# Optimization experiments

Measured on AMD Instinct MI355X. Metric: run time of the kernel, lower is better.

## Reference

```python
import jax, jax.numpy as jnp
import numpy as np

NUM_FIELDS = 24
FIELD_DIM = 2000
VOCAB = NUM_FIELDS * FIELD_DIM  # sum(field_dims) = 48000
EMBED_DIM = 64
H1, H2 = 64, 32
NUM_INTERACTIONS = 16
BATCH = 4096


def setup_inputs() -> dict:
    key = jax.random.key(0)
    ks = jax.random.split(key, 12)
    s = 0.05  # xavier-ish scale
    return {
        "x": jax.random.randint(ks[0], (BATCH, NUM_FIELDS), 0, FIELD_DIM, dtype=jnp.int32),
        # per-field embedding tables stacked: (num_fields, vocab, embed_dim)
        "tables": jax.random.normal(ks[1], (NUM_FIELDS, VOCAB, EMBED_DIM), jnp.float32) * s,
        "fc_w": jax.random.normal(ks[2], (VOCAB, 1), jnp.float32) * s,
        "fc_b": jnp.zeros((1,), jnp.float32),
        "w1": jax.random.normal(ks[3], (2 * EMBED_DIM, H1), jnp.float32) * s,
        "b1": jnp.zeros((H1,), jnp.float32),
        "w2": jax.random.normal(ks[4], (H1, H2), jnp.float32) * s,
        "b2": jnp.zeros((H2,), jnp.float32),
        "w3": jax.random.normal(ks[5], (H2, 1), jnp.float32) * s,
        "b3": jnp.zeros((1,), jnp.float32),
        "proj_w": jax.random.normal(ks[6], (EMBED_DIM, 1), jnp.float32) * s,
        "proj_b": jnp.zeros((1,), jnp.float32),
        "bias": jnp.zeros((1,), jnp.float32),
    }


def reference(x, tables, fc_w, fc_b, w1, b1, w2, b2, w3, b3, proj_w, proj_b, bias):
    offsets = jnp.arange(NUM_FIELDS, dtype=x.dtype) * FIELD_DIM  # cumsum of equal field_dims
    idx = x + offsets[None, :]  # (B, F)

    # FeaturesLinear: first-order term, (B, 1)
    linear_part = fc_w[idx].sum(axis=1) + fc_b

    # FeaturesEmbedding: per-field table lookup -> (B, F, D)
    emb = tables[jnp.arange(NUM_FIELDS)[None, :], idx]

    # FeatureInteractionDetector: all i<j pairs, concat, score with MLP
    iu, ju = jnp.triu_indices(NUM_FIELDS, k=1)  # (P,), P = F*(F-1)/2
    pair_emb = jnp.concatenate([emb[:, iu], emb[:, ju]], axis=-1)  # (B, P, 2D)
    h = jax.nn.relu(pair_emb @ w1 + b1)
    h = jax.nn.relu(h @ w2 + b2)
    scores = (h @ w3 + b3)[..., 0]  # (B, P)

    # topk over batch-mean scores, gather per-sample scores and pair indices
    _, top = jax.lax.top_k(scores.mean(axis=0), NUM_INTERACTIONS)  # (K,)
    sel_scores = scores[:, top]  # (B, K)
    sel_i, sel_j = iu[top], ju[top]

    # FeatureCrossing: elementwise product of selected pairs, score-weighted sum, project
    crossed = emb[:, sel_i] * emb[:, sel_j]  # (B, K, D)
    summed = jnp.sum(crossed * sel_scores[..., None], axis=1)  # (B, D)
    crossed_part = summed @ proj_w + proj_b  # (B, 1)

    out = linear_part + crossed_part + bias  # (B, 1)
    return out[:, 0]
```

## Files before the change

kernel.cpp:

```cpp
#include <hip/hip_runtime.h>
#include <stdint.h>

#define NF 24
#define FD 2000
#define VOCABSZ 48000
#define ED 64
#define H1D 64
#define H2D 32
#define NPAIR 276
#define BATCH 4096
#define NSEL 16
#define NTILE 256
#define PBASE 49152

typedef _Float16 f16x8 __attribute__((ext_vector_type(8)));
typedef _Float16 f16x2 __attribute__((ext_vector_type(2)));
typedef float f32x4 __attribute__((ext_vector_type(4)));

union U4 { f16x8 v; uint32_t u[4]; uint4 q; };
union H2U { f16x2 h; uint32_t u; };

__device__ __forceinline__ uint32_t pkrtz(float lo, float hi){
  uint32_t r; asm("v_cvt_pkrtz_f16_f32 %0, %1, %2" : "=v"(r) : "v"(lo), "v"(hi)); return r;
}
__device__ __forceinline__ uint32_t pk_add(uint32_t a, uint32_t b){
  uint32_t r; asm("v_pk_add_f16 %0, %1, %2" : "=v"(r) : "v"(a), "v"(b)); return r;
}
__device__ __forceinline__ uint32_t pk_mul(uint32_t a, uint32_t b){
  uint32_t r; asm("v_pk_mul_f16 %0, %1, %2" : "=v"(r) : "v"(a), "v"(b)); return r;
}
__device__ __forceinline__ uint32_t pk_relu(uint32_t a){
  uint32_t r; asm("v_pk_max_f16 %0, %1, %2" : "=v"(r) : "v"(a), "v"(0u)); return r;
}
__device__ __forceinline__ float fdot2(uint32_t a, uint32_t b, float c){
  H2U ua, ub; ua.u = a; ub.u = b;
  return __builtin_amdgcn_fdot2(ua.h, ub.h, c, false);
}
#define DPP_ADD(v, ctrl) \
  (v) += __int_as_float(__builtin_amdgcn_update_dpp(0, __float_as_int(v), (ctrl), 0xF, 0xF, true))

__global__ __launch_bounds__(1024) void k_pair(
    const int* __restrict__ x, const float* __restrict__ tables,
    const float* __restrict__ w1, const float* __restrict__ b1,
    const float* __restrict__ w2, const float* __restrict__ b2,
    const float* __restrict__ w3, const float* __restrict__ b3,
    const float* __restrict__ proj_w,
    float* __restrict__ sgT, float* __restrict__ part){
  __shared__ __align__(16) char smem[147456];
  const int tid  = threadIdx.x;
  const int bt   = blockIdx.x;
  const int lane = tid & 63;
  const int w    = tid >> 6;
  const int n    = lane & 15;
  const int kg   = lane >> 4;

  const int half = w >> 3;
  const int oq   = (w >> 1) & 3;
  const int fg   = w & 1;
  const int isPt = (half == 0);
  const float b3v = b3[0];

  const int o = 16*oq + n;
  U4 wp0, wp1;
  {
    const float* wsrc = w1 + (size_t)(isPt ? 0 : ED)*H1D + o;
    #pragma unroll
    for(int j=0;j<8;j++) wp0.v[j] = (_Float16)wsrc[(kg*8+j)*H1D];
    #pragma unroll
    for(int j=0;j<8;j++) wp1.v[j] = (_Float16)wsrc[(32+kg*8+j)*H1D];
  }
  const float b1v = isPt ? b1[o] : 0.f;

  U4 wf[2][2];
  #pragma unroll
  for(int kh=0;kh<2;kh++)
    #pragma unroll
    for(int nh=0;nh<2;nh++)
      #pragma unroll
      for(int q2=0;q2<4;q2++){
        float lo = w2[(kg*8 + 2*q2     + 32*kh)*H2D + n + 16*nh];
        float hi = w2[(kg*8 + 2*q2 + 1 + 32*kh)*H2D + n + 16*nh];
        wf[kh][nh].u[q2] = pkrtz(lo, hi);
      }
  float b2r[2][4], w3r[2][4];
  #pragma unroll
  for(int oh=0;oh<2;oh++)
    #pragma unroll
    for(int r=0;r<4;r++){
      b2r[oh][r] = b2[16*oh + kg*4 + r];
      w3r[oh][r] = w3[16*oh + kg*4 + r];
    }

  uint32_t pw2[8];
  #pragma unroll
  for(int j=0;j<8;j++) pw2[j] = pkrtz(proj_w[kg*16 + 2*j], proj_w[kg*16 + 2*j + 1]);

  #pragma unroll
  for(int i=0;i<3;i++){
    int c = i*1024 + tid;
    int rid = c >> 3;
    int qc = c & 7;
    int f = rid >> 4, b = rid & 15;
    int xv = x[(bt*16 + b)*NF + f];
    const float4* rp = (const float4*)(tables + ((size_t)f*VOCABSZ + (size_t)f*FD + (size_t)xv)*ED + qc*8);
    float4 v0 = rp[0], v1 = rp[1];
    uint4 pk;
    pk.x = pkrtz(v0.x, v0.y); pk.y = pkrtz(v0.z, v0.w);
    pk.z = pkrtz(v1.x, v1.y); pk.w = pkrtz(v1.z, v1.w);
    uint32_t db = ((uint32_t)(f*2048 + b*128 + qc*16)) ^ ((uint32_t)(b&7)<<4);
    *(uint4*)(smem + db) = pk;
  }
  __syncthreads();

  {
    const uint32_t rswz = ((uint32_t)(n&7))<<4;
    const int slab0 = isPt ? 0 : 24;
    for(int ff=0; ff<12; ff++){
      int f = fg*12 + ff;
      U4 a0, a1;
      a0.q = *(const uint4*)(smem + (((uint32_t)(f*2048 + n*128      + kg*16)) ^ rswz));
      a1.q = *(const uint4*)(smem + (((uint32_t)(f*2048 + n*128 + 64 + kg*16)) ^ rswz));
      f32x4 acc = {b1v, b1v, b1v, b1v};
      acc = __builtin_amdgcn_mfma_f32_16x16x32_f16(a0.v, wp0.v, acc, 0,0,0);
      acc = __builtin_amdgcn_mfma_f32_16x16x32_f16(a1.v, wp1.v, acc, 0,0,0);
      int sl = slab0 + f;
      #pragma unroll
      for(int r=0;r<4;r++){
        int bo = kg*4 + r;
        uint32_t db = ((uint32_t)(PBASE + sl*2048 + bo*128 + o*2)) ^ (((uint32_t)(bo&7))<<4);
        *(_Float16*)(smem + db) = (_Float16)acc[r];
      }
    }
  }
  __syncthreads();

  {
    int p0, np;
    if(w < 4){ np = 18; p0 = w*18; } else { np = 17; p0 = 72 + (w-4)*17; }
    int ii = 0, rem = p0;
    while(rem >= (NF-1-ii)){ rem -= (NF-1-ii); ii++; }
    int jj = ii + 1 + rem;

    const uint32_t aswz = ((uint32_t)(n&7))<<4;
    const uint32_t rowoff = (uint32_t)n*128;
    const uint32_t qoff = (uint32_t)kg*16;
    const uint32_t kg32 = (uint32_t)kg*32;

    int cached_i = -1;
    U4 ta0, ta1, ei0, ei1;

    for(int t=0;t<np;t++){
      int p = p0 + t;
      if(ii != cached_i){
        uint32_t tb = (uint32_t)(PBASE + ii*2048) + rowoff;
        ta0.q = *(const uint4*)(smem + ((tb + qoff     ) ^ aswz));
        ta1.q = *(const uint4*)(smem + ((tb + qoff + 64) ^ aswz));
        uint32_t ebi = (uint32_t)(ii*2048) + rowoff + kg32;
        ei0.q = *(const uint4*)(smem + ((ebi     ) ^ aswz));
        ei1.q = *(const uint4*)(smem + ((ebi + 16) ^ aswz));
        cached_i = ii;
      }
      uint32_t ub = (uint32_t)(PBASE + (24+jj)*2048) + rowoff;
      uint4 c0 = *(const uint4*)(smem + ((ub + qoff     ) ^ aswz));
      uint4 c1 = *(const uint4*)(smem + ((ub + qoff + 64) ^ aswz));
      uint32_t ebj = (uint32_t)(jj*2048) + rowoff + kg32;
      U4 ej0, ej1;
      ej0.q = *(const uint4*)(smem + ((ebj     ) ^ aswz));
      ej1.q = *(const uint4*)(smem + ((ebj + 16) ^ aswz));

      U4 h0, h1;
      h0.u[0]=pk_relu(pk_add(ta0.u[0],c0.x)); h0.u[1]=pk_relu(pk_add(ta0.u[1],c0.y));
      h0.u[2]=pk_relu(pk_add(ta0.u[2],c0.z)); h0.u[3]=pk_relu(pk_add(ta0.u[3],c0.w));
      h1.u[0]=pk_relu(pk_add(ta1.u[0],c1.x)); h1.u[1]=pk_relu(pk_add(ta1.u[1],c1.y));
      h1.u[2]=pk_relu(pk_add(ta1.u[2],c1.z)); h1.u[3]=pk_relu(pk_add(ta1.u[3],c1.w));

      f32x4 acc0 = {0.f,0.f,0.f,0.f}, acc1 = {0.f,0.f,0.f,0.f};
      acc0 = __builtin_amdgcn_mfma_f32_16x16x32_f16(wf[0][0].v, h0.v, acc0, 0,0,0);
      acc0 = __builtin_amdgcn_mfma_f32_16x16x32_f16(wf[1][0].v, h1.v, acc0, 0,0,0);
      acc1 = __builtin_amdgcn_mfma_f32_16x16x32_f16(wf[0][1].v, h0.v, acc1, 0,0,0);
      acc1 = __builtin_amdgcn_mfma_f32_16x16x32_f16(wf[1][1].v, h1.v, acc1, 0,0,0);

      float gp = 0.f;
      #pragma unroll
      for(int q=0;q<4;q++) gp = fdot2(pk_mul(ei0.u[q], ej0.u[q]), pw2[q],   gp);
      #pragma unroll
      for(int q=0;q<4;q++) gp = fdot2(pk_mul(ei1.u[q], ej1.u[q]), pw2[4+q], gp);
      gp += __shfl_xor(gp, 16, 64);
      gp += __shfl_xor(gp, 32, 64);

      float tsum = 0.f;
      #pragma unroll
      for(int r=0;r<4;r++){
        float v0 = acc0[r] + b2r[0][r]; v0 = v0>0.f?v0:0.f;
        float v1 = acc1[r] + b2r[1][r]; v1 = v1>0.f?v1:0.f;
        tsum += v0*w3r[0][r] + v1*w3r[1][r];
      }
      tsum += __shfl_xor(tsum, 16, 64);
      tsum += __shfl_xor(tsum, 32, 64);
      float sc = tsum + b3v;

      if(lane < 16) sgT[(size_t)bt*(NPAIR*16) + p*16 + lane] = sc * gp;

      float d = sc;
      DPP_ADD(d, 0x111);
      DPP_ADD(d, 0x112);
      DPP_ADD(d, 0x114);
      DPP_ADD(d, 0x118);
      if(lane == 15) part[(size_t)p*NTILE + bt] = d;

      if(++jj == NF){ ii++; jj = ii+1; }
    }
  }
}

__global__ __launch_bounds__(1024) void k_final(
    const int* __restrict__ x, const float* __restrict__ sgT,
    const float* __restrict__ part,
    const float* __restrict__ fc_w, const float* __restrict__ fc_b,
    const float* __restrict__ proj_b, const float* __restrict__ bias,
    float* __restrict__ out){
  __shared__ float means[NPAIR];
  __shared__ int sel[NSEL];
  int tid = threadIdx.x;
  int bt = blockIdx.x;

  {
    int p = tid >> 2, q = tid & 3;
    const float4* pp = (const float4*)(part + (size_t)p*NTILE + q*64);
    float4 s4 = {0.f,0.f,0.f,0.f};
    #pragma unroll
    for(int i=0;i<16;i++){
      float4 v = pp[i];
      s4.x += v.x; s4.y += v.y; s4.z += v.z; s4.w += v.w;
    }
    float s = (s4.x + s4.y) + (s4.z + s4.w);
    s += __shfl_xor(s, 1, 64);
    s += __shfl_xor(s, 2, 64);
    if(q == 0 && p < 256) means[p] = s;
    if(tid < 80){
      int p2 = 256 + (tid >> 2);
      const float4* pp2 = (const float4*)(part + (size_t)p2*NTILE + q*64);
      float4 t4 = {0.f,0.f,0.f,0.f};
      #pragma unroll
      for(int i=0;i<16;i++){
        float4 v = pp2[i];
        t4.x += v.x; t4.y += v.y; t4.z += v.z; t4.w += v.w;
      }
      float s2 = (t4.x + t4.y) + (t4.z + t4.w);
      s2 += __shfl_xor(s2, 1, 64);
      s2 += __shfl_xor(s2, 2, 64);
      if(q == 0) means[p2] = s2;
    }
  }
  __syncthreads();
  if(tid < 64){
    int l = tid;
    float v[5];
    #pragma unroll
    for(int q=0;q<5;q++){
      int i = l + q*64;
      v[q] = (i < NPAIR) ? means[i] : -3.0e38f;
    }
    for(int s=0;s<NSEL;s++){
      float bv = v[0]; int bslot = 0;
      #pragma unroll
      for(int q=1;q<5;q++){ if(v[q] > bv){ bv = v[q]; bslot = q; } }
      int bi = l + bslot*64;
      float cv = bv; int ci = bi;
      #pragma unroll
      for(int m=1;m<64;m<<=1){
        float ov = __shfl_xor(cv, m, 64);
        int   oi = __shfl_xor(ci, m, 64);
        if(ov > cv || (ov == cv && oi < ci)){ cv = ov; ci = oi; }
      }
      if(l == 0) sel[s] = ci;
      if(bi == ci) v[bslot] = -3.0e38f;
    }
  }
  __syncthreads();

  int row = tid >> 6, lane = tid & 63;
  int brow = bt*16 + row;
  float v = 0.f;
  if(lane < NSEL){
    v = sgT[(size_t)bt*(NPAIR*16) + sel[lane]*16 + row];
  } else if(lane >= 32 && lane < 32+NF){
    int fl = lane - 32;
    v = fc_w[x[brow*NF + fl] + fl*FD];
  }
  #pragma unroll
  for(int m=1;m<64;m<<=1) v += __shfl_xor(v, m, 64);
  if(lane == 0) out[brow] = v + fc_b[0] + proj_b[0] + bias[0];
}

extern "C" void kernel_launch(void* const* d_in, const int* in_sizes, int n_in,
                              void* d_out, int out_size, void* d_ws, size_t ws_size,
                              hipStream_t stream){
  const int*   x      = (const int*)  d_in[0];
  const float* tables = (const float*)d_in[1];
  const float* fc_w   = (const float*)d_in[2];
  const float* fc_b   = (const float*)d_in[3];
  const float* w1     = (const float*)d_in[4];
  const float* b1     = (const float*)d_in[5];
  const float* w2     = (const float*)d_in[6];
  const float* b2     = (const float*)d_in[7];
  const float* w3     = (const float*)d_in[8];
  const float* b3     = (const float*)d_in[9];
  const float* proj_w = (const float*)d_in[10];
  const float* proj_b = (const float*)d_in[11];
  const float* bias   = (const float*)d_in[12];
  float* out = (float*)d_out;

  float* sgT  = (float*)d_ws;
  float* part = sgT + (size_t)NTILE*NPAIR*16;

  k_pair<<<NTILE, 1024, 0, stream>>>(x, tables, w1, b1, w2, b2, w3, b3, proj_w, sgT, part);
  k_final<<<NTILE, 1024, 0, stream>>>(x, sgT, part, fc_w, fc_b, proj_b, bias, out);
}
```

Before: 48.52 us.

## Move linear-term gather into pair kernel and shrink final kernel grid

The first-order fc_w gather and its per-row sum move into k_pair, which already loads x, so the result is written to a small lin buffer. k_final then runs 64 blocks instead of 256, each handling four batch tiles. This cuts the redundant part reduction and top-k that every final block repeats, and drops the fc_w and x gathers from the final kernel. In exchange, k_pair does slightly more work and uses a little more shared memory.

```diff
diff --git a/kernel.cpp b/kernel.cpp
--- a/kernel.cpp
+++ b/kernel.cpp
@@ -12,6 +12,7 @@
 #define NSEL 16
 #define NTILE 256
 #define PBASE 49152
+#define LINB  147456
 
 typedef _Float16 f16x8 __attribute__((ext_vector_type(8)));
 typedef _Float16 f16x2 __attribute__((ext_vector_type(2)));
@@ -44,9 +45,9 @@
     const float* __restrict__ w1, const float* __restrict__ b1,
     const float* __restrict__ w2, const float* __restrict__ b2,
     const float* __restrict__ w3, const float* __restrict__ b3,
-    const float* __restrict__ proj_w,
-    float* __restrict__ sgT, float* __restrict__ part){
-  __shared__ __align__(16) char smem[147456];
+    const float* __restrict__ proj_w, const float* __restrict__ fc_w,
+    float* __restrict__ sgT, float* __restrict__ part, float* __restrict__ lin){
+  __shared__ __align__(16) char smem[148992];
   const int tid  = threadIdx.x;
   const int bt   = blockIdx.x;
   const int lane = tid & 63;
@@ -104,6 +105,7 @@
     int xv = x[(bt*16 + b)*NF + f];
     const float4* rp = (const float4*)(tables + ((size_t)f*VOCABSZ + (size_t)f*FD + (size_t)xv)*ED + qc*8);
     float4 v0 = rp[0], v1 = rp[1];
+    if(qc == 0) *(float*)(smem + LINB + (f*16+b)*4) = fc_w[xv + f*FD];
     uint4 pk;
     pk.x = pkrtz(v0.x, v0.y); pk.y = pkrtz(v0.z, v0.w);
     pk.z = pkrtz(v1.x, v1.y); pk.w = pkrtz(v1.z, v1.w);
@@ -111,6 +113,13 @@
     *(uint4*)(smem + db) = pk;
   }
   __syncthreads();
+
+  if(tid < 16){
+    float s = 0.f;
+    #pragma unroll
+    for(int f=0;f<NF;f++) s += *(const float*)(smem + LINB + (f*16+tid)*4);
+    lin[bt*16 + tid] = s;
+  }
 
   {
     const uint32_t rswz = ((uint32_t)(n&7))<<4;
@@ -214,15 +223,13 @@
 }
 
 __global__ __launch_bounds__(1024) void k_final(
-    const int* __restrict__ x, const float* __restrict__ sgT,
-    const float* __restrict__ part,
-    const float* __restrict__ fc_w, const float* __restrict__ fc_b,
-    const float* __restrict__ proj_b, const float* __restrict__ bias,
-    float* __restrict__ out){
+    const float* __restrict__ sgT, const float* __restrict__ part,
+    const float* __restrict__ lin,
+    const float* __restrict__ fc_b, const float* __restrict__ proj_b,
+    const float* __restrict__ bias, float* __restrict__ out){
   __shared__ float means[NPAIR];
   __shared__ int sel[NSEL];
   int tid = threadIdx.x;
-  int bt = blockIdx.x;
 
   {
     int p = tid >> 2, q = tid & 3;
@@ -279,18 +286,19 @@
   }
   __syncthreads();
 
-  int row = tid >> 6, lane = tid & 63;
-  int brow = bt*16 + row;
-  float v = 0.f;
-  if(lane < NSEL){
-    v = sgT[(size_t)bt*(NPAIR*16) + sel[lane]*16 + row];
-  } else if(lane >= 32 && lane < 32+NF){
-    int fl = lane - 32;
-    v = fc_w[x[brow*NF + fl] + fl*FD];
-  }
-  #pragma unroll
-  for(int m=1;m<64;m<<=1) v += __shfl_xor(v, m, 64);
-  if(lane == 0) out[brow] = v + fc_b[0] + proj_b[0] + bias[0];
+  int wv = tid >> 6, lane = tid & 63;
+  float fcb = fc_b[0], pjb = proj_b[0], bsv = bias[0];
+  #pragma unroll
+  for(int r4=0;r4<4;r4++){
+    int bt = blockIdx.x*4 + r4;
+    int brow = bt*16 + wv;
+    float v = 0.f;
+    if(lane < NSEL)      v = sgT[(size_t)bt*(NPAIR*16) + sel[lane]*16 + wv];
+    else if(lane == 16)  v = lin[brow];
+    #pragma unroll
+    for(int m=1;m<64;m<<=1) v += __shfl_xor(v, m, 64);
+    if(lane == 0) out[brow] = v + fcb + pjb + bsv;
+  }
 }
 
 extern "C" void kernel_launch(void* const* d_in, const int* in_sizes, int n_in,
@@ -313,7 +321,8 @@
 
   float* sgT  = (float*)d_ws;
   float* part = sgT + (size_t)NTILE*NPAIR*16;
-
-  k_pair<<<NTILE, 1024, 0, stream>>>(x, tables, w1, b1, w2, b2, w3, b3, proj_w, sgT, part);
-  k_final<<<NTILE, 1024, 0, stream>>>(x, sgT, part, fc_w, fc_b, proj_b, bias, out);
-}
+  float* lin  = part + (size_t)NPAIR*NTILE;
+
+  k_pair<<<NTILE, 1024, 0, stream>>>(x, tables, w1, b1, w2, b2, w3, b3, proj_w, fc_w, sgT, part, lin);
+  k_final<<<64, 1024, 0, stream>>>(sgT, part, lin, fc_b, proj_b, bias, out);
+}
```

Measured after the change: 51.23 us. +5.6%, slower.
